# Performance work log

Hardware: AMD Instinct MI355X
Metric: run time of the kernel (lower is better)

The kernel has to match this reference:

```python
import jax, jax.numpy as jnp
import numpy as np

HIDDEN = 256
DEPTH = 6
N_MOLS = 5000
ATOMS_PER_MOL = 30
N_ATOMS = N_MOLS * ATOMS_PER_MOL  # 150000 real atoms (+1 padding row)
N_BONDS = 320000                  # directed bonds (+1 padding row)
MAX_NB = 6
ATOM_FDIM = 133
BOND_FDIM = 147


def setup_inputs() -> dict:
    key = jax.random.key(0)
    ks = jax.random.split(key, 8)
    # row 0 of every per-atom / per-bond array is the chemprop zero-padding row
    f_atoms = jax.random.normal(ks[0], (N_ATOMS + 1, ATOM_FDIM), jnp.float32).at[0].set(0.0)
    f_bonds = jax.random.normal(ks[1], (N_BONDS + 1, BOND_FDIM), jnp.float32).at[0].set(0.0)
    a2b = jax.random.randint(ks[2], (N_ATOMS + 1, MAX_NB), 0, N_BONDS + 1, dtype=jnp.int32).at[0].set(0)
    b2a = jax.random.randint(ks[3], (N_BONDS + 1,), 1, N_ATOMS + 1, dtype=jnp.int32).at[0].set(0)
    # directed bonds come in reverse pairs: bond 2k+1 <-> bond 2k+2 (index 0 = pad)
    ids = np.arange(1, N_BONDS + 1)
    rev = ids + np.where(ids % 2 == 1, 1, -1)
    b2revb = jnp.asarray(np.concatenate([[0], rev]), dtype=jnp.int32)
    # contiguous a_scope: molecule i owns atoms [1 + 30*i, 1 + 30*(i+1))
    mol_ids = jnp.repeat(jnp.arange(N_MOLS, dtype=jnp.int32), ATOMS_PER_MOL)
    s = 0.1
    W_i = (jax.random.normal(ks[4], (HIDDEN, BOND_FDIM), jnp.float32) * s)
    W_h = (jax.random.normal(ks[5], (HIDDEN, HIDDEN), jnp.float32) * s)
    W_o = (jax.random.normal(ks[6], (HIDDEN, ATOM_FDIM + HIDDEN), jnp.float32) * s)
    b_o = (jax.random.normal(ks[7], (HIDDEN,), jnp.float32) * s)
    return {"f_atoms": f_atoms, "f_bonds": f_bonds, "a2b": a2b, "b2a": b2a,
            "b2revb": b2revb, "mol_ids": mol_ids,
            "W_i": W_i, "W_h": W_h, "W_o": W_o, "b_o": b_o}


def reference(f_atoms, f_bonds, a2b, b2a, b2revb, mol_ids, W_i, W_h, W_o, b_o):
    # input = W_i(f_bonds) (no bias); message = act(input)
    inp = f_bonds @ W_i.T                       # [B+1, H]
    message = jax.nn.relu(inp)
    for _ in range(DEPTH - 1):
        # gather incoming bond messages per atom, sum over padded neighbor dim
        a_message = message[a2b].sum(axis=1)    # [A+1, H]
        # directed message update: sum at source atom minus reverse message
        message = a_message[b2a] - message[b2revb]  # [B+1, H]
        message = jax.nn.relu(inp + message @ W_h.T)  # dropout p=0 -> identity
    # readout per atom
    a_message = message[a2b].sum(axis=1)        # [A+1, H]
    a_input = jnp.concatenate([f_atoms, a_message], axis=1)  # [A+1, F_a+H]
    atom_hiddens = jax.nn.relu(a_input @ W_o.T + b_o)        # [A+1, H]
    # mean aggregation over each molecule's atoms (a_scope, contiguous, size 30)
    sums = jax.ops.segment_sum(atom_hiddens[1:], mol_ids, num_segments=N_MOLS)
    return sums / float(ATOMS_PER_MOL)
```

## Files before the change

kernel.cpp:

```cpp
#include <hip/hip_runtime.h>
#include <stdint.h>

#define HIDDEN 256
#define NMOLS 5000
#define APM 30
#define NATOMS 150000
#define NBONDS 320000
#define MAXNB 6
#define AFD 133
#define BFD 147
#define A1 (NATOMS + 1)
#define B1 (NBONDS + 1)
#define KI 160
#define KIP 168
#define KO 416

typedef __bf16 bfx8 __attribute__((ext_vector_type(8)));
typedef float fx4 __attribute__((ext_vector_type(4)));
typedef unsigned short u16x8 __attribute__((ext_vector_type(8)));

__device__ __forceinline__ float b2f(unsigned short u) {
    union { unsigned int i; float f; } v; v.i = ((unsigned int)u) << 16; return v.f;
}
__device__ __forceinline__ unsigned short f2b(float f) {
    union { float f; unsigned int i; } v; v.f = f;
    unsigned int r = v.i + 0x7FFFu + ((v.i >> 16) & 1u);
    return (unsigned short)(r >> 16);
}

__global__ void k_convw(const float* __restrict__ Wi, const float* __restrict__ Wh,
                        const float* __restrict__ Wo,
                        unsigned short* __restrict__ wi, unsigned short* __restrict__ wh,
                        unsigned short* __restrict__ wo) {
    int t = blockIdx.x * 256 + threadIdx.x;
    if (t < 256 * KI) {
        int n = t / KI, k = t % KI;
        wi[t] = (k < BFD) ? f2b(Wi[n * BFD + k]) : (unsigned short)0;
        return;
    }
    int t2 = t - 256 * KI;
    if (t2 < 256 * 256) {
        wh[t2] = f2b(Wh[t2]);
        return;
    }
    int t3 = t2 - 256 * 256;
    if (t3 < 256 * KO) {
        int n = t3 / KO, k = t3 % KO;
        float v = 0.f;
        if (k < AFD) v = Wo[n * (AFD + HIDDEN) + k];
        else if (k >= 160) v = Wo[n * (AFD + HIDDEN) + AFD + (k - 160)];
        wo[t3] = f2b(v);
    }
}

__global__ __launch_bounds__(256) void k_gemm_wi(
    const float* __restrict__ fb, const unsigned short* __restrict__ wi,
    unsigned short* __restrict__ inp)
{
    __shared__ float s_f32[64 * BFD];
    __shared__ unsigned short s_bf[64 * KIP];
    const int m0 = blockIdx.x * 64;
    const int tid = threadIdx.x;

    {
        const size_t base = (size_t)m0 * BFD;
        const size_t tot = (size_t)B1 * BFD;
        const float4* src4 = (const float4*)(fb + base);
#pragma unroll
        for (int i = 0; i < 10; ++i) {
            const int t4 = i * 256 + tid;
            if (t4 < (64 * BFD) / 4) {
                const size_t f = base + (size_t)t4 * 4;
                float4 v;
                if (f + 4 <= tot) {
                    v = src4[t4];
                } else {
                    v.x = (f + 0 < tot) ? fb[f + 0] : 0.f;
                    v.y = (f + 1 < tot) ? fb[f + 1] : 0.f;
                    v.z = (f + 2 < tot) ? fb[f + 2] : 0.f;
                    v.w = (f + 3 < tot) ? fb[f + 3] : 0.f;
                }
                *(float4*)(s_f32 + t4 * 4) = v;
            }
        }
    }
    __syncthreads();

    {
        const int r = tid >> 2, p = tid & 3;
        const float* srow = s_f32 + r * BFD;
        unsigned short* drow = s_bf + r * KIP;
#pragma unroll
        for (int i = 0; i < 5; ++i) {
            const int c0 = (i * 4 + p) * 8;
            u16x8 o;
#pragma unroll
            for (int e = 0; e < 8; ++e) {
                float v = (c0 + e < BFD) ? srow[c0 + e] : 0.f;
                o[e] = f2b(v);
            }
            *(u16x8*)(drow + c0) = o;
        }
    }
    __syncthreads();

    const int wv = tid >> 6, ln = tid & 63;
    const int l15 = ln & 15, lhi = ln >> 4;
    fx4 acc[4][4];
#pragma unroll
    for (int a = 0; a < 4; ++a)
#pragma unroll
        for (int b = 0; b < 4; ++b)
#pragma unroll
            for (int q = 0; q < 4; ++q) acc[a][b][q] = 0.f;

#pragma unroll
    for (int ks = 0; ks < 5; ++ks) {
        const int kk = ks * 32 + lhi * 8;
        bfx8 af[4], bb[4];
#pragma unroll
        for (int mf = 0; mf < 4; ++mf) {
            const int rr = mf * 16 + l15;
            af[mf] = *(const bfx8*)(s_bf + rr * KIP + kk);
        }
#pragma unroll
        for (int nf = 0; nf < 4; ++nf) {
            const int n = wv * 64 + nf * 16 + l15;
            bb[nf] = *(const bfx8*)(wi + n * KI + kk);
        }
#pragma unroll
        for (int mf = 0; mf < 4; ++mf)
#pragma unroll
            for (int nf = 0; nf < 4; ++nf)
                acc[mf][nf] = __builtin_amdgcn_mfma_f32_16x16x32_bf16(af[mf], bb[nf], acc[mf][nf], 0, 0, 0);
    }
    const int cb = wv * 64 + l15;
    const int rb = lhi * 4;
#pragma unroll
    for (int mf = 0; mf < 4; ++mf) {
#pragma unroll
        for (int j = 0; j < 4; ++j) {
            const int g = m0 + mf * 16 + rb + j;
            if (g < B1) {
#pragma unroll
                for (int nf = 0; nf < 4; ++nf) {
                    inp[(size_t)g * HIDDEN + cb + nf * 16] = f2b(acc[mf][nf][j]);
                }
            }
        }
    }
}

__global__ __launch_bounds__(256) void k_gather(
    const unsigned short* __restrict__ msg, const int* __restrict__ a2b,
    unsigned short* __restrict__ amsg, const int relu_src)
{
    const int gt = blockIdx.x * 256 + threadIdx.x;
    const int atom = gt >> 5;
    const int s = gt & 31;
    if (atom >= A1) return;
    const int* nb = a2b + atom * MAXNB;
    float acc[8];
#pragma unroll
    for (int e = 0; e < 8; ++e) acc[e] = 0.f;
#pragma unroll
    for (int j = 0; j < MAXNB; ++j) {
        const int b = nb[j];
        u16x8 v = *(const u16x8*)(msg + (size_t)b * HIDDEN + s * 8);
#pragma unroll
        for (int e = 0; e < 8; ++e) {
            float x = b2f(v[e]);
            if (relu_src) x = x > 0.f ? x : 0.f;
            acc[e] += x;
        }
    }
    u16x8 o;
#pragma unroll
    for (int e = 0; e < 8; ++e) o[e] = f2b(acc[e]);
    *(u16x8*)(amsg + (size_t)atom * HIDDEN + s * 8) = o;
}

__global__ __launch_bounds__(256) void k_gemm_wh(
    const unsigned short* __restrict__ amsg,
    const unsigned short* __restrict__ msgp,
    const int* __restrict__ b2a, const int* __restrict__ b2revb,
    const unsigned short* __restrict__ wh,
    const unsigned short* __restrict__ inp,
    unsigned short* __restrict__ msgn, const int relu_rev)
{
    __shared__ unsigned short lds[64 * 256];
    const int m0 = blockIdx.x * 64;
    const int tid = threadIdx.x;
    {
        const int r = tid >> 2, p = tid & 3;
        const int b = m0 + r;
        const bool ok = (b < B1);
        int i1 = 0, i2 = 0;
        if (ok) { i1 = b2a[b]; i2 = b2revb[b]; }
        const unsigned short* s1 = amsg + (size_t)i1 * HIDDEN;
        const unsigned short* s2 = msgp + (size_t)i2 * HIDDEN;
        char* ldsrow = (char*)lds + r * 512;
        const int sw = (r & 7) << 4;
#pragma unroll
        for (int i = 0; i < 8; ++i) {
            const int slot = i * 4 + p;
            const int c0 = slot * 8;
            u16x8 o;
            if (ok) {
                u16x8 a = *(const u16x8*)(s1 + c0);
                u16x8 m = *(const u16x8*)(s2 + c0);
#pragma unroll
                for (int e = 0; e < 8; ++e) {
                    float mv = b2f(m[e]);
                    if (relu_rev) mv = mv > 0.f ? mv : 0.f;
                    o[e] = f2b(b2f(a[e]) - mv);
                }
            } else {
#pragma unroll
                for (int e = 0; e < 8; ++e) o[e] = 0;
            }
            *(u16x8*)(ldsrow + ((slot * 16) ^ sw)) = o;
        }
    }
    __syncthreads();

    const int wv = tid >> 6, ln = tid & 63;
    const int l15 = ln & 15, lhi = ln >> 4;
    fx4 acc[4][4];
#pragma unroll
    for (int a = 0; a < 4; ++a)
#pragma unroll
        for (int b = 0; b < 4; ++b)
#pragma unroll
            for (int q = 0; q < 4; ++q) acc[a][b][q] = 0.f;

#pragma unroll
    for (int ks = 0; ks < 8; ++ks) {
        const int kk = ks * 32 + lhi * 8;
        bfx8 af[4], bb[4];
#pragma unroll
        for (int mf = 0; mf < 4; ++mf) {
            const int rr = mf * 16 + l15;
            af[mf] = *(const bfx8*)((const char*)lds + rr * 512 + ((kk * 2) ^ ((rr & 7) << 4)));
        }
#pragma unroll
        for (int nf = 0; nf < 4; ++nf) {
            const int n = wv * 64 + nf * 16 + l15;
            bb[nf] = *(const bfx8*)(wh + n * 256 + kk);
        }
#pragma unroll
        for (int mf = 0; mf < 4; ++mf)
#pragma unroll
            for (int nf = 0; nf < 4; ++nf)
                acc[mf][nf] = __builtin_amdgcn_mfma_f32_16x16x32_bf16(af[mf], bb[nf], acc[mf][nf], 0, 0, 0);
    }
    const int cb = wv * 64 + l15;
    const int rb = lhi * 4;
#pragma unroll
    for (int mf = 0; mf < 4; ++mf) {
#pragma unroll
        for (int j = 0; j < 4; ++j) {
            const int g = m0 + mf * 16 + rb + j;
            if (g < B1) {
#pragma unroll
                for (int nf = 0; nf < 4; ++nf) {
                    const size_t idx = (size_t)g * HIDDEN + cb + nf * 16;
                    float v = b2f(inp[idx]) + acc[mf][nf][j];
                    msgn[idx] = f2b(v > 0.f ? v : 0.f);
                }
            }
        }
    }
}

__global__ __launch_bounds__(256) void k_gemm_wo(
    const float* __restrict__ fa,
    const unsigned short* __restrict__ amsg,
    const unsigned short* __restrict__ wo,
    const float* __restrict__ bo,
    unsigned short* __restrict__ ah)
{
    __shared__ unsigned short lds[64 * KO];
    const int m0 = blockIdx.x * 64;
    const int tid = threadIdx.x;
    {
        const int r = tid >> 2, p = tid & 3;
        const int a = m0 + r;
        const bool ok = (a < A1);
        const float* src = fa + (size_t)a * AFD;
        unsigned short* drow = lds + r * KO;
#pragma unroll
        for (int i = 0; i < 13; ++i) {
            const int c0 = (i * 4 + p) * 8;
            u16x8 o;
            if (ok && c0 + 8 <= AFD) {
#pragma unroll
                for (int e = 0; e < 8; ++e) o[e] = f2b(src[c0 + e]);
            } else if (ok && c0 < AFD) {
#pragma unroll
                for (int e = 0; e < 8; ++e) o[e] = (c0 + e < AFD) ? f2b(src[c0 + e]) : (unsigned short)0;
            } else if (ok && c0 >= 160) {
                o = *(const u16x8*)(amsg + (size_t)a * HIDDEN + (c0 - 160));
            } else {
#pragma unroll
                for (int e = 0; e < 8; ++e) o[e] = 0;
            }
            *(u16x8*)(drow + c0) = o;
        }
    }
    __syncthreads();

    const int wv = tid >> 6, ln = tid & 63;
    const int l15 = ln & 15, lhi = ln >> 4;
    fx4 acc[4][4];
#pragma unroll
    for (int a = 0; a < 4; ++a)
#pragma unroll
        for (int b = 0; b < 4; ++b)
#pragma unroll
            for (int q = 0; q < 4; ++q) acc[a][b][q] = 0.f;

#pragma unroll
    for (int ks = 0; ks < 13; ++ks) {
        const int kk = ks * 32 + lhi * 8;
        bfx8 af[4], bb[4];
#pragma unroll
        for (int mf = 0; mf < 4; ++mf) {
            const int rr = mf * 16 + l15;
            af[mf] = *(const bfx8*)(lds + rr * KO + kk);
        }
#pragma unroll
        for (int nf = 0; nf < 4; ++nf) {
            const int n = wv * 64 + nf * 16 + l15;
            bb[nf] = *(const bfx8*)(wo + n * KO + kk);
        }
#pragma unroll
        for (int mf = 0; mf < 4; ++mf)
#pragma unroll
            for (int nf = 0; nf < 4; ++nf)
                acc[mf][nf] = __builtin_amdgcn_mfma_f32_16x16x32_bf16(af[mf], bb[nf], acc[mf][nf], 0, 0, 0);
    }
    const int cb = wv * 64 + l15;
    const int rb = lhi * 4;
    float bias[4];
#pragma unroll
    for (int nf = 0; nf < 4; ++nf) bias[nf] = bo[cb + nf * 16];
#pragma unroll
    for (int mf = 0; mf < 4; ++mf) {
#pragma unroll
        for (int j = 0; j < 4; ++j) {
            const int g = m0 + mf * 16 + rb + j;
            if (g < A1) {
#pragma unroll
                for (int nf = 0; nf < 4; ++nf) {
                    float v = acc[mf][nf][j] + bias[nf];
                    ah[(size_t)g * HIDDEN + cb + nf * 16] = f2b(v > 0.f ? v : 0.f);
                }
            }
        }
    }
}

__global__ __launch_bounds__(256) void k_pool(const unsigned short* __restrict__ ah,
                                              float* __restrict__ out) {
    const int mol = blockIdx.x;
    const int h = threadIdx.x;
    const unsigned short* base = ah + ((size_t)(1 + mol * APM)) * HIDDEN + h;
    float s = 0.f;
#pragma unroll
    for (int i = 0; i < APM; ++i) s += b2f(base[(size_t)i * HIDDEN]);
    out[(size_t)mol * HIDDEN + h] = s * (1.0f / APM);
}

extern "C" void kernel_launch(void* const* d_in, const int* in_sizes, int n_in,
                              void* d_out, int out_size, void* d_ws, size_t ws_size,
                              hipStream_t stream)
{
    const float* f_atoms = (const float*)d_in[0];
    const float* f_bonds = (const float*)d_in[1];
    const int* a2b    = (const int*)d_in[2];
    const int* b2a    = (const int*)d_in[3];
    const int* b2revb = (const int*)d_in[4];
    const float* W_i  = (const float*)d_in[6];
    const float* W_h  = (const float*)d_in[7];
    const float* W_o  = (const float*)d_in[8];
    const float* b_o  = (const float*)d_in[9];
    float* out = (float*)d_out;

    char* ws = (char*)d_ws;
    size_t off = 0;
    auto alloc = [&](size_t n) { char* p = ws + off; off = (off + n + 255) & ~(size_t)255; return p; };
    unsigned short* wi   = (unsigned short*)alloc((size_t)256 * KI * 2);
    unsigned short* wh   = (unsigned short*)alloc((size_t)256 * 256 * 2);
    unsigned short* wo   = (unsigned short*)alloc((size_t)256 * KO * 2);
    unsigned short* inp  = (unsigned short*)alloc((size_t)B1 * HIDDEN * 2);
    unsigned short* msgA = (unsigned short*)alloc((size_t)B1 * HIDDEN * 2);
    unsigned short* msgB = (unsigned short*)alloc((size_t)B1 * HIDDEN * 2);
    unsigned short* amsg = (unsigned short*)alloc((size_t)A1 * HIDDEN * 2);
    unsigned short* ah = inp;

    k_convw<<<832, 256, 0, stream>>>(W_i, W_h, W_o, wi, wh, wo);

    const int gb = (B1 + 63) / 64;
    const int ga = (A1 + 63) / 64;
    const int gg = (A1 * 32 + 255) / 256;

    k_gemm_wi<<<gb, 256, 0, stream>>>(f_bonds, wi, inp);

    k_gather<<<gg, 256, 0, stream>>>(inp, a2b, amsg, 1);
    k_gemm_wh<<<gb, 256, 0, stream>>>(amsg, inp, b2a, b2revb, wh, inp, msgA, 1);

    unsigned short* cur = msgA;
    unsigned short* nxt = msgB;
    for (int it = 1; it < 5; ++it) {
        k_gather<<<gg, 256, 0, stream>>>(cur, a2b, amsg, 0);
        k_gemm_wh<<<gb, 256, 0, stream>>>(amsg, cur, b2a, b2revb, wh, inp, nxt, 0);
        unsigned short* t = cur; cur = nxt; nxt = t;
    }
    k_gather<<<gg, 256, 0, stream>>>(cur, a2b, amsg, 0);
    k_gemm_wo<<<ga, 256, 0, stream>>>(f_atoms, amsg, wo, b_o, ah);
    k_pool<<<NMOLS, 256, 0, stream>>>(ah, out);
}
```

Before: 1.674 ms.

## Fold subtraction into K-concatenated GEMM, stage epilogues through LDS for coalesced stores

The W_h kernel no longer computes a_msg[b2a]-msg[b2revb] elementwise. It copies both gathered rows, with the reverse one sign-flipped, into a 512-wide K tile and runs a doubled-K GEMM over 32-row tiles, which avoids one bf16 rounding and the per-element conversions. The W_i kernel also writes a ReLU'd copy of the input so the gather and W_h kernels drop their relu flags. All GEMM epilogues now stage results through swizzled LDS and write 16-byte coalesced rows instead of scattered 2-byte stores. The price is twice the MFMA work per bond row and extra LDS round trips and barriers.

```diff
diff --git a/kernel.cpp b/kernel.cpp
--- a/kernel.cpp
+++ b/kernel.cpp
@@ -18,6 +18,7 @@
 typedef __bf16 bfx8 __attribute__((ext_vector_type(8)));
 typedef float fx4 __attribute__((ext_vector_type(4)));
 typedef unsigned short u16x8 __attribute__((ext_vector_type(8)));
+typedef unsigned int u32x4 __attribute__((ext_vector_type(4)));
 
 __device__ __forceinline__ float b2f(unsigned short u) {
     union { unsigned int i; float f; } v; v.i = ((unsigned int)u) << 16; return v.f;
@@ -55,7 +56,7 @@
 
 __global__ __launch_bounds__(256) void k_gemm_wi(
     const float* __restrict__ fb, const unsigned short* __restrict__ wi,
-    unsigned short* __restrict__ inp)
+    unsigned short* __restrict__ inp, unsigned short* __restrict__ msg0)
 {
     __shared__ float s_f32[64 * BFD];
     __shared__ unsigned short s_bf[64 * KIP];
@@ -134,26 +135,46 @@
             for (int nf = 0; nf < 4; ++nf)
                 acc[mf][nf] = __builtin_amdgcn_mfma_f32_16x16x32_bf16(af[mf], bb[nf], acc[mf][nf], 0, 0, 0);
     }
-    const int cb = wv * 64 + l15;
-    const int rb = lhi * 4;
-#pragma unroll
-    for (int mf = 0; mf < 4; ++mf) {
-#pragma unroll
-        for (int j = 0; j < 4; ++j) {
-            const int g = m0 + mf * 16 + rb + j;
-            if (g < B1) {
+
+    __syncthreads();
+    unsigned short* cbuf = (unsigned short*)s_f32;
+    {
+        const int cb = wv * 64 + l15;
+        const int rb = lhi * 4;
+#pragma unroll
+        for (int mf = 0; mf < 4; ++mf)
+#pragma unroll
+            for (int j = 0; j < 4; ++j) {
+                const int row = mf * 16 + rb + j;
 #pragma unroll
                 for (int nf = 0; nf < 4; ++nf) {
-                    inp[(size_t)g * HIDDEN + cb + nf * 16] = f2b(acc[mf][nf][j]);
+                    const int col = cb + nf * 16;
+                    const int byte = (row * 512) + (((col * 2) & ~15) ^ ((row & 7) << 4)) + ((col * 2) & 15);
+                    *(unsigned short*)((char*)cbuf + byte) = f2b(acc[mf][nf][j]);
                 }
             }
+    }
+    __syncthreads();
+#pragma unroll
+    for (int i = 0; i < 8; ++i) {
+        const int row = i * 8 + (tid >> 5);
+        const int col16 = tid & 31;
+        const int byte = row * 512 + ((col16 * 16) ^ ((row & 7) << 4));
+        u16x8 c = *(const u16x8*)((const char*)cbuf + byte);
+        const int g = m0 + row;
+        if (g < B1) {
+            u16x8 m;
+#pragma unroll
+            for (int e = 0; e < 8; ++e) m[e] = (c[e] & 0x8000u) ? (unsigned short)0 : c[e];
+            *(u16x8*)(inp + (size_t)g * HIDDEN + col16 * 8) = c;
+            *(u16x8*)(msg0 + (size_t)g * HIDDEN + col16 * 8) = m;
         }
     }
 }
 
 __global__ __launch_bounds__(256) void k_gather(
     const unsigned short* __restrict__ msg, const int* __restrict__ a2b,
-    unsigned short* __restrict__ amsg, const int relu_src)
+    unsigned short* __restrict__ amsg)
 {
     const int gt = blockIdx.x * 256 + threadIdx.x;
     const int atom = gt >> 5;
@@ -168,11 +189,7 @@
         const int b = nb[j];
         u16x8 v = *(const u16x8*)(msg + (size_t)b * HIDDEN + s * 8);
 #pragma unroll
-        for (int e = 0; e < 8; ++e) {
-            float x = b2f(v[e]);
-            if (relu_src) x = x > 0.f ? x : 0.f;
-            acc[e] += x;
-        }
+        for (int e = 0; e < 8; ++e) acc[e] += b2f(v[e]);
     }
     u16x8 o;
 #pragma unroll
@@ -186,62 +203,53 @@
     const int* __restrict__ b2a, const int* __restrict__ b2revb,
     const unsigned short* __restrict__ wh,
     const unsigned short* __restrict__ inp,
-    unsigned short* __restrict__ msgn, const int relu_rev)
+    unsigned short* __restrict__ msgn)
 {
-    __shared__ unsigned short lds[64 * 256];
-    const int m0 = blockIdx.x * 64;
+    __shared__ unsigned short lds[32 * 512];
+    const int m0 = blockIdx.x * 32;
     const int tid = threadIdx.x;
-    {
-        const int r = tid >> 2, p = tid & 3;
+
+    {
+        const int r = tid >> 3, p = tid & 7;
         const int b = m0 + r;
         const bool ok = (b < B1);
         int i1 = 0, i2 = 0;
         if (ok) { i1 = b2a[b]; i2 = b2revb[b]; }
-        const unsigned short* s1 = amsg + (size_t)i1 * HIDDEN;
-        const unsigned short* s2 = msgp + (size_t)i2 * HIDDEN;
-        char* ldsrow = (char*)lds + r * 512;
+        const u32x4* s1 = (const u32x4*)(amsg + (size_t)i1 * HIDDEN);
+        const u32x4* s2 = (const u32x4*)(msgp + (size_t)i2 * HIDDEN);
+        char* base = (char*)lds + r * 1024;
         const int sw = (r & 7) << 4;
 #pragma unroll
-        for (int i = 0; i < 8; ++i) {
-            const int slot = i * 4 + p;
-            const int c0 = slot * 8;
-            u16x8 o;
-            if (ok) {
-                u16x8 a = *(const u16x8*)(s1 + c0);
-                u16x8 m = *(const u16x8*)(s2 + c0);
-#pragma unroll
-                for (int e = 0; e < 8; ++e) {
-                    float mv = b2f(m[e]);
-                    if (relu_rev) mv = mv > 0.f ? mv : 0.f;
-                    o[e] = f2b(b2f(a[e]) - mv);
-                }
-            } else {
-#pragma unroll
-                for (int e = 0; e < 8; ++e) o[e] = 0;
-            }
-            *(u16x8*)(ldsrow + ((slot * 16) ^ sw)) = o;
+        for (int c = 0; c < 4; ++c) {
+            const int ch = c * 8 + p;
+            u32x4 va = ok ? s1[ch] : (u32x4)(0u);
+            *(u32x4*)(base + ((ch * 16) ^ sw)) = va;
+            u32x4 vm = ok ? s2[ch] : (u32x4)(0u);
+            vm ^= 0x80008000u;
+            *(u32x4*)(base + (512 + ((ch * 16) ^ sw))) = vm;
         }
     }
     __syncthreads();
 
     const int wv = tid >> 6, ln = tid & 63;
     const int l15 = ln & 15, lhi = ln >> 4;
-    fx4 acc[4][4];
-#pragma unroll
-    for (int a = 0; a < 4; ++a)
+    fx4 acc[2][4];
+#pragma unroll
+    for (int a = 0; a < 2; ++a)
 #pragma unroll
         for (int b = 0; b < 4; ++b)
 #pragma unroll
             for (int q = 0; q < 4; ++q) acc[a][b][q] = 0.f;
 
 #pragma unroll
-    for (int ks = 0; ks < 8; ++ks) {
-        const int kk = ks * 32 + lhi * 8;
-        bfx8 af[4], bb[4];
-#pragma unroll
-        for (int mf = 0; mf < 4; ++mf) {
+    for (int ks = 0; ks < 16; ++ks) {
+        const int sect = ks >> 3, k8 = ks & 7;
+        const int kk = k8 * 32 + lhi * 8;
+        bfx8 af[2], bb[4];
+#pragma unroll
+        for (int mf = 0; mf < 2; ++mf) {
             const int rr = mf * 16 + l15;
-            af[mf] = *(const bfx8*)((const char*)lds + rr * 512 + ((kk * 2) ^ ((rr & 7) << 4)));
+            af[mf] = *(const bfx8*)((const char*)lds + rr * 1024 + sect * 512 + ((kk * 2) ^ ((rr & 7) << 4)));
         }
 #pragma unroll
         for (int nf = 0; nf < 4; ++nf) {
@@ -249,26 +257,47 @@
             bb[nf] = *(const bfx8*)(wh + n * 256 + kk);
         }
 #pragma unroll
-        for (int mf = 0; mf < 4; ++mf)
+        for (int mf = 0; mf < 2; ++mf)
 #pragma unroll
             for (int nf = 0; nf < 4; ++nf)
                 acc[mf][nf] = __builtin_amdgcn_mfma_f32_16x16x32_bf16(af[mf], bb[nf], acc[mf][nf], 0, 0, 0);
     }
-    const int cb = wv * 64 + l15;
-    const int rb = lhi * 4;
-#pragma unroll
-    for (int mf = 0; mf < 4; ++mf) {
-#pragma unroll
-        for (int j = 0; j < 4; ++j) {
-            const int g = m0 + mf * 16 + rb + j;
-            if (g < B1) {
+
+    __syncthreads();
+    {
+        const int cb = wv * 64 + l15;
+        const int rb = lhi * 4;
+#pragma unroll
+        for (int mf = 0; mf < 2; ++mf)
+#pragma unroll
+            for (int j = 0; j < 4; ++j) {
+                const int row = mf * 16 + rb + j;
 #pragma unroll
                 for (int nf = 0; nf < 4; ++nf) {
-                    const size_t idx = (size_t)g * HIDDEN + cb + nf * 16;
-                    float v = b2f(inp[idx]) + acc[mf][nf][j];
-                    msgn[idx] = f2b(v > 0.f ? v : 0.f);
+                    const int col = cb + nf * 16;
+                    const int byte = (row * 512) + (((col * 2) & ~15) ^ ((row & 7) << 4)) + ((col * 2) & 15);
+                    *(unsigned short*)((char*)lds + byte) = f2b(acc[mf][nf][j]);
                 }
             }
+    }
+    __syncthreads();
+#pragma unroll
+    for (int i = 0; i < 4; ++i) {
+        const int row = i * 8 + (tid >> 5);
+        const int col16 = tid & 31;
+        const int byte = row * 512 + ((col16 * 16) ^ ((row & 7) << 4));
+        u16x8 c = *(const u16x8*)((const char*)lds + byte);
+        const int g = m0 + row;
+        if (g < B1) {
+            const size_t off = (size_t)g * HIDDEN + col16 * 8;
+            u16x8 ip = *(const u16x8*)(inp + off);
+            u16x8 o;
+#pragma unroll
+            for (int e = 0; e < 8; ++e) {
+                float v = b2f(ip[e]) + b2f(c[e]);
+                o[e] = f2b(v > 0.f ? v : 0.f);
+            }
+            *(u16x8*)(msgn + off) = o;
         }
     }
 }
@@ -340,23 +369,42 @@
             for (int nf = 0; nf < 4; ++nf)
                 acc[mf][nf] = __builtin_amdgcn_mfma_f32_16x16x32_bf16(af[mf], bb[nf], acc[mf][nf], 0, 0, 0);
     }
-    const int cb = wv * 64 + l15;
-    const int rb = lhi * 4;
-    float bias[4];
-#pragma unroll
-    for (int nf = 0; nf < 4; ++nf) bias[nf] = bo[cb + nf * 16];
-#pragma unroll
-    for (int mf = 0; mf < 4; ++mf) {
-#pragma unroll
-        for (int j = 0; j < 4; ++j) {
-            const int g = m0 + mf * 16 + rb + j;
-            if (g < A1) {
+
+    __syncthreads();
+    {
+        const int cb = wv * 64 + l15;
+        const int rb = lhi * 4;
+#pragma unroll
+        for (int mf = 0; mf < 4; ++mf)
+#pragma unroll
+            for (int j = 0; j < 4; ++j) {
+                const int row = mf * 16 + rb + j;
 #pragma unroll
                 for (int nf = 0; nf < 4; ++nf) {
-                    float v = acc[mf][nf][j] + bias[nf];
-                    ah[(size_t)g * HIDDEN + cb + nf * 16] = f2b(v > 0.f ? v : 0.f);
+                    const int col = cb + nf * 16;
+                    const int byte = (row * 512) + (((col * 2) & ~15) ^ ((row & 7) << 4)) + ((col * 2) & 15);
+                    *(unsigned short*)((char*)lds + byte) = f2b(acc[mf][nf][j]);
                 }
             }
+    }
+    __syncthreads();
+#pragma unroll
+    for (int i = 0; i < 8; ++i) {
+        const int row = i * 8 + (tid >> 5);
+        const int col16 = tid & 31;
+        const int byte = row * 512 + ((col16 * 16) ^ ((row & 7) << 4));
+        u16x8 c = *(const u16x8*)((const char*)lds + byte);
+        const int g = m0 + row;
+        if (g < A1) {
+            fx4 bi0 = *(const fx4*)(bo + col16 * 8);
+            fx4 bi1 = *(const fx4*)(bo + col16 * 8 + 4);
+            u16x8 o;
+#pragma unroll
+            for (int e = 0; e < 8; ++e) {
+                float v = b2f(c[e]) + (e < 4 ? bi0[e] : bi1[e - 4]);
+                o[e] = f2b(v > 0.f ? v : 0.f);
+            }
+            *(u16x8*)(ah + (size_t)g * HIDDEN + col16 * 8) = o;
         }
     }
 }
@@ -401,23 +449,21 @@
 
     k_convw<<<832, 256, 0, stream>>>(W_i, W_h, W_o, wi, wh, wo);
 
-    const int gb = (B1 + 63) / 64;
+    const int gb64 = (B1 + 63) / 64;
+    const int gb32 = (B1 + 31) / 32;
     const int ga = (A1 + 63) / 64;
     const int gg = (A1 * 32 + 255) / 256;
 
-    k_gemm_wi<<<gb, 256, 0, stream>>>(f_bonds, wi, inp);
-
-    k_gather<<<gg, 256, 0, stream>>>(inp, a2b, amsg, 1);
-    k_gemm_wh<<<gb, 256, 0, stream>>>(amsg, inp, b2a, b2revb, wh, inp, msgA, 1);
-
-    unsigned short* cur = msgA;
-    unsigned short* nxt = msgB;
-    for (int it = 1; it < 5; ++it) {
-        k_gather<<<gg, 256, 0, stream>>>(cur, a2b, amsg, 0);
-        k_gemm_wh<<<gb, 256, 0, stream>>>(amsg, cur, b2a, b2revb, wh, inp, nxt, 0);
+    k_gemm_wi<<<gb64, 256, 0, stream>>>(f_bonds, wi, inp, msgB);
+
+    unsigned short* cur = msgB;
+    unsigned short* nxt = msgA;
+    for (int it = 0; it < 5; ++it) {
+        k_gather<<<gg, 256, 0, stream>>>(cur, a2b, amsg);
+        k_gemm_wh<<<gb32, 256, 0, stream>>>(amsg, cur, b2a, b2revb, wh, inp, nxt);
         unsigned short* t = cur; cur = nxt; nxt = t;
     }
-    k_gather<<<gg, 256, 0, stream>>>(cur, a2b, amsg, 0);
+    k_gather<<<gg, 256, 0, stream>>>(cur, a2b, amsg);
     k_gemm_wo<<<ga, 256, 0, stream>>>(f_atoms, amsg, wo, b_o, ah);
     k_pool<<<NMOLS, 256, 0, stream>>>(ah, out);
 }
```

Measured after the change: 2.249 ms. 34.3% more time.
